# Performance work log

Hardware: AMD Instinct MI355X
Metric: run time of the kernel (lower is better)

## Reference

```python
import jax, jax.numpy as jnp
import numpy as np

NUM_HEADS = 8
QUERY_DIM = 512
VALUE_DIM = 512
INPUT_DIM = 512
Q_HEAD = QUERY_DIM // NUM_HEADS   # 64
V_HEAD = VALUE_DIM // NUM_HEADS   # 64
TOPK = 5
BN_EPS = 1e-5


def setup_inputs() -> dict:
    key = jax.random.key(0)
    ks = jax.random.split(key, 3)
    B = 2048
    x = jax.random.normal(ks[0], (B, INPUT_DIM), dtype=jnp.float32)
    # small init scale so softmax logits are reasonable
    W_qkv = jax.random.normal(ks[1], (INPUT_DIM, 2 * QUERY_DIM + VALUE_DIM), dtype=jnp.float32) * 0.02
    W_proj = jax.random.normal(ks[2], (VALUE_DIM, VALUE_DIM), dtype=jnp.float32) * 0.02
    b_proj = jnp.zeros((VALUE_DIM,), dtype=jnp.float32)
    bn_gamma = jnp.ones((VALUE_DIM,), dtype=jnp.float32)
    bn_beta = jnp.zeros((VALUE_DIM,), dtype=jnp.float32)
    return {"x": x, "W_qkv": W_qkv, "W_proj": W_proj, "b_proj": b_proj,
            "bn_gamma": bn_gamma, "bn_beta": bn_beta}


def _batchnorm_train(y, gamma, beta):
    # torch BatchNorm1d training mode: batch mean, biased variance
    mean = y.mean(axis=0)
    var = y.var(axis=0)  # biased (ddof=0), matches torch normalization
    return gamma * (y - mean) * jax.lax.rsqrt(var + BN_EPS) + beta


def reference(x, W_qkv, W_proj, b_proj, bn_gamma, bn_beta):
    B = x.shape[0]
    # qkv_transform: Linear(input_dim, 2Q + V, bias=False)
    qkv = x @ W_qkv                                   # [B, 2Q+V]
    qv = qkv[:, :2 * QUERY_DIM].reshape(B, 2, NUM_HEADS, Q_HEAD)
    q = qv[:, 0].transpose(1, 0, 2)                   # [H, B, hd]
    k = qv[:, 1].transpose(1, 0, 2)                   # [H, B, hd]
    v = qkv[:, 2 * QUERY_DIM:].reshape(B, NUM_HEADS, V_HEAD).transpose(1, 0, 2)  # [H, B, vd]

    scale = 1.0 / jnp.sqrt(jnp.float32(Q_HEAD))
    logits = jnp.einsum('hqd,hkd->hqk', q, k) * scale  # [H, B, B]
    attn = jax.nn.softmax(logits, axis=-1)

    # per-head: zero the top-5 columns by summed attention weight (no grad through selection)
    col_sums = jax.lax.stop_gradient(attn.sum(axis=1))           # [H, B]
    _, top_idx = jax.lax.top_k(col_sums, TOPK)                   # [H, 5]
    mask = jnp.ones((NUM_HEADS, B), dtype=attn.dtype)
    mask = mask.at[jnp.arange(NUM_HEADS)[:, None], top_idx].set(0.0)
    attn = attn * mask[:, None, :]                               # zero columns

    out = jnp.einsum('hqk,hkd->hqd', attn, v)                    # [H, B, vd]
    out = out.transpose(1, 0, 2).reshape(B, VALUE_DIM)
    # proj: Linear + BatchNorm1d (training mode) + ReLU
    out = out @ W_proj.T + b_proj
    out = jax.nn.relu(_batchnorm_train(out, bn_gamma, bn_beta))
    return out, attn
```

## Files before the change

kernel.cpp:

```cpp
#include <hip/hip_runtime.h>
#include <hip/hip_bf16.h>

#define B 2048
#define NH 8
#define HD 64
#define DIM 512
#define QKVN 1536
#define OUT0_ELEMS ((size_t)B * DIM)

typedef float f32x4 __attribute__((ext_vector_type(4)));
typedef __bf16 bf16x8 __attribute__((ext_vector_type(8)));

static __device__ __forceinline__ unsigned short f2bf(float f) {
    unsigned int u = __builtin_bit_cast(unsigned int, f);
    u += 0x7fffu + ((u >> 16) & 1u);
    return (unsigned short)(u >> 16);
}
static __device__ __forceinline__ float bfhi2f(unsigned int u) {
    return __builtin_bit_cast(float, u & 0xffff0000u);
}
static __device__ __forceinline__ float bflo2f(unsigned int u) {
    return __builtin_bit_cast(float, u << 16);
}

__global__ __launch_bounds__(256) void prep_cast(const float* __restrict__ x,
                                                 const float* __restrict__ wp,
                                                 const float* __restrict__ wqkv,
                                                 unsigned short* __restrict__ xbf,
                                                 unsigned short* __restrict__ wpbf,
                                                 unsigned short* __restrict__ wT) {
    int bx = blockIdx.x;
    int tid = threadIdx.x;
    if (bx < 1280) {
        size_t t = (size_t)bx * 256 + tid;
        const float4* src;
        ushort4* dst;
        size_t idx;
        if (t < 262144) { src = (const float4*)x; dst = (ushort4*)xbf; idx = t; }
        else            { src = (const float4*)wp; dst = (ushort4*)wpbf; idx = t - 262144; }
        float4 v = src[idx];
        ushort4 u;
        u.x = f2bf(v.x); u.y = f2bf(v.y); u.z = f2bf(v.z); u.w = f2bf(v.w);
        dst[idx] = u;
        return;
    }
    int b = bx - 1280;
    int n0 = (b % 24) * 64;
    int k0 = (b / 24) * 64;
    __shared__ unsigned short T[64][72];
#pragma unroll
    for (int it = 0; it < 4; ++it) {
        int chunk = it * 256 + tid;
        int r = chunk >> 4, c4 = (chunk & 15) * 4;
        float4 v = *(const float4*)(wqkv + (size_t)(k0 + r) * QKVN + n0 + c4);
        T[c4 + 0][r] = f2bf(v.x); T[c4 + 1][r] = f2bf(v.y);
        T[c4 + 2][r] = f2bf(v.z); T[c4 + 3][r] = f2bf(v.w);
    }
    __syncthreads();
#pragma unroll
    for (int it = 0; it < 2; ++it) {
        int chunk = it * 256 + tid;
        int r = chunk >> 3, c8 = (chunk & 7) * 8;
        ushort4 u0, u1;
        u0.x = T[r][c8 + 0]; u0.y = T[r][c8 + 1]; u0.z = T[r][c8 + 2]; u0.w = T[r][c8 + 3];
        u1.x = T[r][c8 + 4]; u1.y = T[r][c8 + 5]; u1.z = T[r][c8 + 6]; u1.w = T[r][c8 + 7];
        *(ushort4*)(wT + (size_t)(n0 + r) * 512 + k0 + c8) = u0;
        *(ushort4*)(wT + (size_t)(n0 + r) * 512 + k0 + c8 + 4) = u1;
    }
}

__global__ __launch_bounds__(256) void gemm_qkv_mfma(const unsigned short* __restrict__ xbf,
                                                     const unsigned short* __restrict__ wT,
                                                     float* __restrict__ v_f32,
                                                     unsigned short* __restrict__ qkbf,
                                                     unsigned short* __restrict__ vT) {
    int nt = blockIdx.x;
    int mt = blockIdx.y;
    __shared__ uint4 Ax[128 * 8];
    __shared__ uint4 Bw[64 * 8];
    int tid = threadIdx.x;
    int l = tid & 63, wid = tid >> 6;
    int wr = wid >> 1, wc = wid & 1;
    const uint4* x4 = (const uint4*)xbf;
    const uint4* w4 = (const uint4*)wT;
    f32x4 acc[4][2];
#pragma unroll
    for (int i = 0; i < 4; ++i)
#pragma unroll
        for (int j = 0; j < 2; ++j) acc[i][j] = (f32x4){0.f, 0.f, 0.f, 0.f};

    for (int kt = 0; kt < 8; ++kt) {
        int kg = kt * 8;
#pragma unroll
        for (int it = 0; it < 4; ++it) {
            int chunk = it * 256 + tid;
            int row = chunk >> 3, slot = chunk & 7;
            Ax[row * 8 + (slot ^ (row & 7))] = x4[(size_t)(mt * 128 + row) * 64 + kg + slot];
        }
#pragma unroll
        for (int it = 0; it < 2; ++it) {
            int chunk = it * 256 + tid;
            int row = chunk >> 3, slot = chunk & 7;
            Bw[row * 8 + (slot ^ (row & 7))] = w4[(size_t)(nt * 64 + row) * 64 + kg + slot];
        }
        __syncthreads();
#pragma unroll
        for (int km = 0; km < 2; ++km) {
            int gsel = km * 4 + (l >> 4);
            bf16x8 a[4], b[2];
#pragma unroll
            for (int i = 0; i < 4; ++i) {
                int row = wr * 64 + i * 16 + (l & 15);
                a[i] = __builtin_bit_cast(bf16x8, Ax[row * 8 + (gsel ^ (row & 7))]);
            }
#pragma unroll
            for (int j = 0; j < 2; ++j) {
                int row = wc * 32 + j * 16 + (l & 15);
                b[j] = __builtin_bit_cast(bf16x8, Bw[row * 8 + (gsel ^ (row & 7))]);
            }
#pragma unroll
            for (int i = 0; i < 4; ++i)
#pragma unroll
                for (int j = 0; j < 2; ++j)
                    acc[i][j] = __builtin_amdgcn_mfma_f32_16x16x32_bf16(a[i], b[j], acc[i][j], 0, 0, 0);
        }
        __syncthreads();
    }
    if (nt < 16) {
#pragma unroll
        for (int i = 0; i < 4; ++i)
#pragma unroll
            for (int j = 0; j < 2; ++j)
#pragma unroll
                for (int reg = 0; reg < 4; ++reg) {
                    int row = mt * 128 + wr * 64 + i * 16 + (l >> 4) * 4 + reg;
                    int col = nt * 64 + wc * 32 + j * 16 + (l & 15);
                    qkbf[(size_t)row * 1024 + col] = f2bf(acc[i][j][reg]);
                }
    } else {
        int h = nt - 16;
#pragma unroll
        for (int i = 0; i < 4; ++i)
#pragma unroll
            for (int j = 0; j < 2; ++j) {
                int k0r = mt * 128 + wr * 64 + i * 16 + (l >> 4) * 4;
                int d = wc * 32 + j * 16 + (l & 15);
                uint2 pk;
                pk.x = (unsigned)f2bf(acc[i][j][0]) | ((unsigned)f2bf(acc[i][j][1]) << 16);
                pk.y = (unsigned)f2bf(acc[i][j][2]) | ((unsigned)f2bf(acc[i][j][3]) << 16);
                *(uint2*)(vT + ((size_t)(h * 64 + d) * 2048 + k0r)) = pk;
#pragma unroll
                for (int reg = 0; reg < 4; ++reg)
                    v_f32[(size_t)(k0r + reg) * DIM + h * 64 + d] = acc[i][j][reg];
            }
    }
}

template<int PHASE>
__global__ __launch_bounds__(256) void attn_pass(const unsigned short* __restrict__ qkbf,
                                                 const unsigned short* __restrict__ vT,
                                                 const float* __restrict__ rowsum_in,
                                                 float* __restrict__ rowsum_out,
                                                 float* __restrict__ attn,
                                                 float* __restrict__ colsum,
                                                 float* __restrict__ ovp) {
    int ct = blockIdx.x, qt = blockIdx.y, h = blockIdx.z;
    int tid = threadIdx.x;
    int l = tid & 63;
    int wid = tid >> 6;
    int wr = wid >> 1;
    int wc = wid & 1;

    __shared__ uint4 Qs[128 * 8];
    __shared__ uint4 Ks[64 * 8];
    __shared__ uint4 Vt[64 * 8];
    __shared__ uint4 Pl4[128 * 8];
    __shared__ float cs[512];
    __shared__ float rinv[128];
    unsigned short* Pl = (unsigned short*)Pl4;

    const uint4* src = (const uint4*)qkbf;
#pragma unroll
    for (int it = 0; it < 4; ++it) {
        int chunk = it * 256 + tid;
        int row = chunk >> 3, slot = chunk & 7;
        Qs[row * 8 + (slot ^ (row & 7))] = src[(size_t)(qt * 128 + row) * 128 + h * 8 + slot];
    }
    if constexpr (PHASE == 2) {
        if (tid < 128) rinv[tid] = 1.0f / rowsum_in[h * B + qt * 128 + tid];
        if (tid < 256) { cs[tid] = 0.f; cs[tid + 256] = 0.f; }
    }

    float rsum[4][4];
    f32x4 O[4][2];
    if constexpr (PHASE == 1) {
#pragma unroll
        for (int i = 0; i < 4; ++i)
#pragma unroll
            for (int r = 0; r < 4; ++r) rsum[i][r] = 0.f;
    } else {
#pragma unroll
        for (int i = 0; i < 4; ++i)
#pragma unroll
            for (int j = 0; j < 2; ++j) O[i][j] = (f32x4){0.f, 0.f, 0.f, 0.f};
    }

    size_t hbb = (size_t)h * B * B;
    for (int sub = 0; sub < 8; ++sub) {
        int kbase = ct * 512 + sub * 64;
#pragma unroll
        for (int it = 0; it < 2; ++it) {
            int chunk = it * 256 + tid;
            int row = chunk >> 3, slot = chunk & 7;
            Ks[row * 8 + (slot ^ (row & 7))] = src[(size_t)(kbase + row) * 128 + 64 + h * 8 + slot];
        }
        if constexpr (PHASE == 2) {
#pragma unroll
            for (int it = 0; it < 2; ++it) {
                int chunk = it * 256 + tid;
                int d = chunk >> 3, g = chunk & 7;
                Vt[d * 8 + (g ^ (d & 7))] =
                    *(const uint4*)(vT + ((size_t)(h * 64 + d) * 2048 + kbase + g * 8));
            }
        }
        __syncthreads();

        f32x4 S[4][2];
#pragma unroll
        for (int i = 0; i < 4; ++i)
#pragma unroll
            for (int j = 0; j < 2; ++j) S[i][j] = (f32x4){0.f, 0.f, 0.f, 0.f};
#pragma unroll
        for (int km = 0; km < 2; ++km) {
            int gsel = km * 4 + (l >> 4);
            bf16x8 aq[4], bk[2];
#pragma unroll
            for (int i = 0; i < 4; ++i) {
                int row = wr * 64 + i * 16 + (l & 15);
                aq[i] = __builtin_bit_cast(bf16x8, Qs[row * 8 + (gsel ^ (row & 7))]);
            }
#pragma unroll
            for (int j = 0; j < 2; ++j) {
                int row = wc * 32 + j * 16 + (l & 15);
                bk[j] = __builtin_bit_cast(bf16x8, Ks[row * 8 + (gsel ^ (row & 7))]);
            }
#pragma unroll
            for (int i = 0; i < 4; ++i)
#pragma unroll
                for (int j = 0; j < 2; ++j)
                    S[i][j] = __builtin_amdgcn_mfma_f32_16x16x32_bf16(aq[i], bk[j], S[i][j], 0, 0, 0);
        }

        if constexpr (PHASE == 1) {
#pragma unroll
            for (int i = 0; i < 4; ++i)
#pragma unroll
                for (int j = 0; j < 2; ++j)
#pragma unroll
                    for (int reg = 0; reg < 4; ++reg)
                        rsum[i][reg] += __expf(S[i][j][reg] * 0.125f);
            __syncthreads();
        } else {
            float csacc[2] = {0.f, 0.f};
#pragma unroll
            for (int i = 0; i < 4; ++i) {
#pragma unroll
                for (int j = 0; j < 2; ++j) {
                    int kcol = wc * 32 + j * 16 + (l & 15);
#pragma unroll
                    for (int reg = 0; reg < 4; ++reg) {
                        int qrow = wr * 64 + i * 16 + (l >> 4) * 4 + reg;
                        float p = __expf(S[i][j][reg] * 0.125f) * rinv[qrow];
                        csacc[j] += p;
                        Pl[qrow * 64 + ((kcol & 7) | ((((kcol >> 3) ^ (qrow & 7))) << 3))] = f2bf(p);
                    }
                }
            }
#pragma unroll
            for (int j = 0; j < 2; ++j) {
                float v = csacc[j];
                v += __shfl_xor(v, 16);
                v += __shfl_xor(v, 32);
                if (l < 16) atomicAdd(&cs[sub * 64 + wc * 32 + j * 16 + l], v);
            }
            __syncthreads();
#pragma unroll
            for (int it2 = 0; it2 < 4; ++it2) {
                int chunk = it2 * 256 + tid;
                int row = chunk >> 3, g = chunk & 7;
                uint4 pv = Pl4[row * 8 + (g ^ (row & 7))];
                float4 lo, hi;
                lo.x = bflo2f(pv.x); lo.y = bfhi2f(pv.x);
                lo.z = bflo2f(pv.y); lo.w = bfhi2f(pv.y);
                hi.x = bflo2f(pv.z); hi.y = bfhi2f(pv.z);
                hi.z = bflo2f(pv.w); hi.w = bfhi2f(pv.w);
                float* dst = attn + hbb + (size_t)(qt * 128 + row) * B + kbase + g * 8;
                *(float4*)dst = lo;
                *(float4*)(dst + 4) = hi;
            }
#pragma unroll
            for (int km = 0; km < 2; ++km) {
                int gsel = km * 4 + (l >> 4);
                bf16x8 pa[4], vb[2];
#pragma unroll
                for (int i = 0; i < 4; ++i) {
                    int q = wr * 64 + i * 16 + (l & 15);
                    pa[i] = __builtin_bit_cast(bf16x8, Pl4[q * 8 + (gsel ^ (q & 7))]);
                }
#pragma unroll
                for (int j = 0; j < 2; ++j) {
                    int d = wc * 32 + j * 16 + (l & 15);
                    vb[j] = __builtin_bit_cast(bf16x8, Vt[d * 8 + (gsel ^ (d & 7))]);
                }
#pragma unroll
                for (int i = 0; i < 4; ++i)
#pragma unroll
                    for (int j = 0; j < 2; ++j)
                        O[i][j] = __builtin_amdgcn_mfma_f32_16x16x32_bf16(pa[i], vb[j], O[i][j], 0, 0, 0);
            }
            __syncthreads();
        }
    }

    if constexpr (PHASE == 1) {
#pragma unroll
        for (int i = 0; i < 4; ++i)
#pragma unroll
            for (int reg = 0; reg < 4; ++reg) {
                float v = rsum[i][reg];
                v += __shfl_xor(v, 1); v += __shfl_xor(v, 2);
                v += __shfl_xor(v, 4); v += __shfl_xor(v, 8);
                if ((l & 15) == 0)
                    atomicAdd(&rowsum_out[h * B + qt * 128 + wr * 64 + i * 16 + (l >> 4) * 4 + reg], v);
            }
    } else {
        for (int i = tid; i < 512; i += 256)
            atomicAdd(&colsum[h * B + ct * 512 + i], cs[i]);
#pragma unroll
        for (int i = 0; i < 4; ++i)
#pragma unroll
            for (int j = 0; j < 2; ++j)
#pragma unroll
                for (int reg = 0; reg < 4; ++reg) {
                    int qrow = wr * 64 + i * 16 + (l >> 4) * 4 + reg;
                    ovp[((size_t)ct * B + qt * 128 + qrow) * DIM + h * 64 + wc * 32 + j * 16 + (l & 15)] =
                        O[i][j][reg];
                }
    }
}

__global__ __launch_bounds__(256) void maskfix_topk(float* __restrict__ attn,
                                                    const float* __restrict__ v_f32,
                                                    const float* __restrict__ colsum,
                                                    const float* __restrict__ ovp,
                                                    unsigned short* __restrict__ ovbf) {
    int rt = blockIdx.x;
    int h = blockIdx.y;
    int tid = threadIdx.x;
    __shared__ float v[B];
    __shared__ float bv[256];
    __shared__ int bi[256];
    __shared__ float Pl[5][64];
    __shared__ float Vl[5][64];
    __shared__ int tix[5];
    for (int i = tid; i < B; i += 256) v[i] = colsum[h * B + i];
    __syncthreads();
    for (int it = 0; it < 5; ++it) {
        float best = -1e30f;
        int bidx = 0;
        for (int i = tid; i < B; i += 256) {
            float x = v[i];
            if (x > best || (x == best && i < bidx)) { best = x; bidx = i; }
        }
        bv[tid] = best; bi[tid] = bidx;
        __syncthreads();
        for (int s = 128; s > 0; s >>= 1) {
            if (tid < s) {
                if (bv[tid + s] > bv[tid] ||
                    (bv[tid + s] == bv[tid] && bi[tid + s] < bi[tid])) {
                    bv[tid] = bv[tid + s]; bi[tid] = bi[tid + s];
                }
            }
            __syncthreads();
        }
        if (tid == 0) { tix[it] = bi[0]; v[bi[0]] = -1e30f; }
        __syncthreads();
    }
    size_t abase = (size_t)h * B * B + (size_t)(rt * 64) * B;
    for (int t = tid; t < 320; t += 256) {
        int i = t / 64, q = t % 64;
        Pl[i][q] = attn[abase + (size_t)q * B + tix[i]];
        Vl[i][q] = v_f32[(size_t)tix[i] * DIM + h * 64 + q];
    }
    __syncthreads();
    for (int t = tid; t < 320; t += 256) {
        int i = t / 64, q = t % 64;
        attn[abase + (size_t)q * B + tix[i]] = 0.f;
    }
    int tx = tid % 16, ty = tid / 16;
    float corr[4][4] = {};
#pragma unroll
    for (int i = 0; i < 5; ++i)
#pragma unroll
        for (int a = 0; a < 4; ++a)
#pragma unroll
            for (int b2 = 0; b2 < 4; ++b2)
                corr[a][b2] += Pl[i][ty * 4 + a] * Vl[i][tx * 4 + b2];
#pragma unroll
    for (int a = 0; a < 4; ++a) {
        size_t row = (size_t)(rt * 64 + ty * 4 + a);
        size_t col = h * 64 + tx * 4;
        float4 s0 = *(const float4*)(ovp + ((size_t)0 * B + row) * DIM + col);
        float4 s1 = *(const float4*)(ovp + ((size_t)1 * B + row) * DIM + col);
        float4 s2 = *(const float4*)(ovp + ((size_t)2 * B + row) * DIM + col);
        float4 s3 = *(const float4*)(ovp + ((size_t)3 * B + row) * DIM + col);
        ushort4 u;
        u.x = f2bf(s0.x + s1.x + s2.x + s3.x - corr[a][0]);
        u.y = f2bf(s0.y + s1.y + s2.y + s3.y - corr[a][1]);
        u.z = f2bf(s0.z + s1.z + s2.z + s3.z - corr[a][2]);
        u.w = f2bf(s0.w + s1.w + s2.w + s3.w - corr[a][3]);
        *(ushort4*)(ovbf + row * DIM + col) = u;
    }
}

__global__ __launch_bounds__(256) void proj_gemm_mfma(const unsigned short* __restrict__ ovbf,
                                                      const unsigned short* __restrict__ wpbf,
                                                      const float* __restrict__ bproj,
                                                      float* __restrict__ y,
                                                      float* __restrict__ sums,
                                                      float* __restrict__ ssums) {
    int nt = blockIdx.x;
    int mt = blockIdx.y;
    __shared__ uint4 Ax[128 * 8];
    __shared__ uint4 Bw[64 * 8];
    __shared__ float sb[64];
    __shared__ float qb[64];
    int tid = threadIdx.x;
    int l = tid & 63, wid = tid >> 6;
    int wr = wid >> 1, wc = wid & 1;
    if (tid < 64) { sb[tid] = 0.f; qb[tid] = 0.f; }
    const uint4* a4 = (const uint4*)ovbf;
    const uint4* b4 = (const uint4*)wpbf;
    f32x4 acc[4][2];
#pragma unroll
    for (int i = 0; i < 4; ++i)
#pragma unroll
        for (int j = 0; j < 2; ++j) acc[i][j] = (f32x4){0.f, 0.f, 0.f, 0.f};

    for (int kt = 0; kt < 8; ++kt) {
        int kg = kt * 8;
#pragma unroll
        for (int it = 0; it < 4; ++it) {
            int chunk = it * 256 + tid;
            int row = chunk >> 3, slot = chunk & 7;
            Ax[row * 8 + (slot ^ (row & 7))] = a4[(size_t)(mt * 128 + row) * 64 + kg + slot];
        }
#pragma unroll
        for (int it = 0; it < 2; ++it) {
            int chunk = it * 256 + tid;
            int row = chunk >> 3, slot = chunk & 7;
            Bw[row * 8 + (slot ^ (row & 7))] = b4[(size_t)(nt * 64 + row) * 64 + kg + slot];
        }
        __syncthreads();
#pragma unroll
        for (int km = 0; km < 2; ++km) {
            int gsel = km * 4 + (l >> 4);
            bf16x8 a[4], b[2];
#pragma unroll
            for (int i = 0; i < 4; ++i) {
                int row = wr * 64 + i * 16 + (l & 15);
                a[i] = __builtin_bit_cast(bf16x8, Ax[row * 8 + (gsel ^ (row & 7))]);
            }
#pragma unroll
            for (int j = 0; j < 2; ++j) {
                int row = wc * 32 + j * 16 + (l & 15);
                b[j] = __builtin_bit_cast(bf16x8, Bw[row * 8 + (gsel ^ (row & 7))]);
            }
#pragma unroll
            for (int i = 0; i < 4; ++i)
#pragma unroll
                for (int j = 0; j < 2; ++j)
                    acc[i][j] = __builtin_amdgcn_mfma_f32_16x16x32_bf16(a[i], b[j], acc[i][j], 0, 0, 0);
        }
        __syncthreads();
    }
    float ls[2] = {0.f, 0.f};
    float lq[2] = {0.f, 0.f};
#pragma unroll
    for (int i = 0; i < 4; ++i)
#pragma unroll
        for (int j = 0; j < 2; ++j) {
            int col = nt * 64 + wc * 32 + j * 16 + (l & 15);
            float bp = bproj[col];
#pragma unroll
            for (int reg = 0; reg < 4; ++reg) {
                int row = mt * 128 + wr * 64 + i * 16 + (l >> 4) * 4 + reg;
                float c = acc[i][j][reg] + bp;
                y[(size_t)row * DIM + col] = c;
                ls[j] += c; lq[j] += c * c;
            }
        }
#pragma unroll
    for (int j = 0; j < 2; ++j) {
        atomicAdd(&sb[wc * 32 + j * 16 + (l & 15)], ls[j]);
        atomicAdd(&qb[wc * 32 + j * 16 + (l & 15)], lq[j]);
    }
    __syncthreads();
    if (tid < 64) {
        atomicAdd(&sums[nt * 64 + tid], sb[tid]);
        atomicAdd(&ssums[nt * 64 + tid], qb[tid]);
    }
}

__global__ __launch_bounds__(256) void bn_apply(const float* __restrict__ y,
                                                const float* __restrict__ sums,
                                                const float* __restrict__ ssums,
                                                const float* __restrict__ gamma,
                                                const float* __restrict__ beta,
                                                float* __restrict__ out) {
    int t = blockIdx.x * 256 + threadIdx.x;
    int c4 = (t % 128) * 4;
    size_t r = t / 128;
    if (r >= B) return;
    float4 s = *(const float4*)(sums + c4);
    float4 q = *(const float4*)(ssums + c4);
    float4 m, rs;
    m.x = s.x * (1.0f / B); m.y = s.y * (1.0f / B);
    m.z = s.z * (1.0f / B); m.w = s.w * (1.0f / B);
    rs.x = rsqrtf(q.x * (1.0f / B) - m.x * m.x + 1e-5f);
    rs.y = rsqrtf(q.y * (1.0f / B) - m.y * m.y + 1e-5f);
    rs.z = rsqrtf(q.z * (1.0f / B) - m.z * m.z + 1e-5f);
    rs.w = rsqrtf(q.w * (1.0f / B) - m.w * m.w + 1e-5f);
    float4 v = *(const float4*)(y + r * DIM + c4);
    float4 g = *(const float4*)(gamma + c4);
    float4 bt = *(const float4*)(beta + c4);
    float4 o;
    o.x = fmaxf(0.f, g.x * (v.x - m.x) * rs.x + bt.x);
    o.y = fmaxf(0.f, g.y * (v.y - m.y) * rs.y + bt.y);
    o.z = fmaxf(0.f, g.z * (v.z - m.z) * rs.z + bt.z);
    o.w = fmaxf(0.f, g.w * (v.w - m.w) * rs.w + bt.w);
    *(float4*)(out + r * DIM + c4) = o;
}

extern "C" void kernel_launch(void* const* d_in, const int* in_sizes, int n_in,
                              void* d_out, int out_size, void* d_ws, size_t ws_size,
                              hipStream_t stream) {
    const float* x = (const float*)d_in[0];
    const float* W_qkv = (const float*)d_in[1];
    const float* W_proj = (const float*)d_in[2];
    const float* b_proj = (const float*)d_in[3];
    const float* bn_gamma = (const float*)d_in[4];
    const float* bn_beta = (const float*)d_in[5];

    float* out0 = (float*)d_out;
    float* attn = (float*)d_out + OUT0_ELEMS;

    float* ws = (float*)d_ws;
    float* v_f32 = ws;
    float* ovp = v_f32 + OUT0_ELEMS;
    float* y = ovp + 4 * OUT0_ELEMS;
    float* rowsum = y + OUT0_ELEMS;
    float* colsum = rowsum + NH * B;
    float* sums = colsum + NH * B;
    float* ssums = sums + DIM;
    unsigned short* qkbf = (unsigned short*)(ssums + DIM);
    unsigned short* vT = qkbf + (size_t)B * 1024;
    unsigned short* wpbf = vT + (size_t)NH * HD * B;
    unsigned short* ovbf = wpbf + (size_t)DIM * DIM;
    unsigned short* xbf = (unsigned short*)ovp;
    unsigned short* wT = xbf + (size_t)B * 512;

    hipMemsetAsync(rowsum, 0, (2 * NH * B + 2 * DIM) * sizeof(float), stream);

    prep_cast<<<1280 + 192, 256, 0, stream>>>(x, W_proj, W_qkv, xbf, wpbf, wT);
    gemm_qkv_mfma<<<dim3(QKVN / 64, B / 128), 256, 0, stream>>>(xbf, wT, v_f32, qkbf, vT);
    attn_pass<1><<<dim3(4, 16, NH), 256, 0, stream>>>(qkbf, vT, nullptr, rowsum,
                                                      attn, colsum, ovp);
    attn_pass<2><<<dim3(4, 16, NH), 256, 0, stream>>>(qkbf, vT, rowsum, nullptr,
                                                      attn, colsum, ovp);
    maskfix_topk<<<dim3(B / 64, NH), 256, 0, stream>>>(attn, v_f32, colsum, ovp, ovbf);
    proj_gemm_mfma<<<dim3(DIM / 64, B / 128), 256, 0, stream>>>(ovbf, wpbf, b_proj,
                                                                y, sums, ssums);
    bn_apply<<<(B * DIM / 4 + 255) / 256, 256, 0, stream>>>(y, sums, ssums,
                                                            bn_gamma, bn_beta, out0);
}
```

Before: 104.5 us.

## Split attention passes into finer-grained grids and fold memset into prep kernel

The templated two-phase attention kernel becomes two separate kernels. The rowsum pass now covers 256 key columns per block, doubling its grid. The second pass works on 64-row query tiles with one 16-column slice per wave, doubling that grid and cutting shared memory per block. The zeroing of rowsum/colsum/sums buffers moves from a hipMemsetAsync into extra blocks of prep_cast, saving one launch. More blocks should raise occupancy and fill the GPU better, but K/V tiles are reloaded more often and there are more atomics.

```diff
diff --git a/kernel.cpp b/kernel.cpp
--- a/kernel.cpp
+++ b/kernel.cpp
@@ -28,7 +28,8 @@
                                                  const float* __restrict__ wqkv,
                                                  unsigned short* __restrict__ xbf,
                                                  unsigned short* __restrict__ wpbf,
-                                                 unsigned short* __restrict__ wT) {
+                                                 unsigned short* __restrict__ wT,
+                                                 float* __restrict__ zero_region) {
     int bx = blockIdx.x;
     int tid = threadIdx.x;
     if (bx < 1280) {
@@ -42,6 +43,12 @@
         ushort4 u;
         u.x = f2bf(v.x); u.y = f2bf(v.y); u.z = f2bf(v.z); u.w = f2bf(v.w);
         dst[idx] = u;
+        return;
+    }
+    if (bx >= 1472) {
+        int idx = (bx - 1472) * 256 + tid;
+        if (idx < 8448)
+            ((float4*)zero_region)[idx] = make_float4(0.f, 0.f, 0.f, 0.f);
         return;
     }
     int b = bx - 1280;
@@ -156,14 +163,8 @@
     }
 }
 
-template<int PHASE>
-__global__ __launch_bounds__(256) void attn_pass(const unsigned short* __restrict__ qkbf,
-                                                 const unsigned short* __restrict__ vT,
-                                                 const float* __restrict__ rowsum_in,
-                                                 float* __restrict__ rowsum_out,
-                                                 float* __restrict__ attn,
-                                                 float* __restrict__ colsum,
-                                                 float* __restrict__ ovp) {
+__global__ __launch_bounds__(256) void attn_rowsum(const unsigned short* __restrict__ qkbf,
+                                                   float* __restrict__ rowsum) {
     int ct = blockIdx.x, qt = blockIdx.y, h = blockIdx.z;
     int tid = threadIdx.x;
     int l = tid & 63;
@@ -173,11 +174,6 @@
 
     __shared__ uint4 Qs[128 * 8];
     __shared__ uint4 Ks[64 * 8];
-    __shared__ uint4 Vt[64 * 8];
-    __shared__ uint4 Pl4[128 * 8];
-    __shared__ float cs[512];
-    __shared__ float rinv[128];
-    unsigned short* Pl = (unsigned short*)Pl4;
 
     const uint4* src = (const uint4*)qkbf;
 #pragma unroll
@@ -186,43 +182,21 @@
         int row = chunk >> 3, slot = chunk & 7;
         Qs[row * 8 + (slot ^ (row & 7))] = src[(size_t)(qt * 128 + row) * 128 + h * 8 + slot];
     }
-    if constexpr (PHASE == 2) {
-        if (tid < 128) rinv[tid] = 1.0f / rowsum_in[h * B + qt * 128 + tid];
-        if (tid < 256) { cs[tid] = 0.f; cs[tid + 256] = 0.f; }
-    }
 
     float rsum[4][4];
-    f32x4 O[4][2];
-    if constexpr (PHASE == 1) {
-#pragma unroll
-        for (int i = 0; i < 4; ++i)
-#pragma unroll
-            for (int r = 0; r < 4; ++r) rsum[i][r] = 0.f;
-    } else {
-#pragma unroll
-        for (int i = 0; i < 4; ++i)
-#pragma unroll
-            for (int j = 0; j < 2; ++j) O[i][j] = (f32x4){0.f, 0.f, 0.f, 0.f};
-    }
-
-    size_t hbb = (size_t)h * B * B;
-    for (int sub = 0; sub < 8; ++sub) {
-        int kbase = ct * 512 + sub * 64;
+#pragma unroll
+    for (int i = 0; i < 4; ++i)
+#pragma unroll
+        for (int r = 0; r < 4; ++r) rsum[i][r] = 0.f;
+
+    for (int sub = 0; sub < 4; ++sub) {
+        int kbase = ct * 256 + sub * 64;
 #pragma unroll
         for (int it = 0; it < 2; ++it) {
             int chunk = it * 256 + tid;
             int row = chunk >> 3, slot = chunk & 7;
             Ks[row * 8 + (slot ^ (row & 7))] = src[(size_t)(kbase + row) * 128 + 64 + h * 8 + slot];
         }
-        if constexpr (PHASE == 2) {
-#pragma unroll
-            for (int it = 0; it < 2; ++it) {
-                int chunk = it * 256 + tid;
-                int d = chunk >> 3, g = chunk & 7;
-                Vt[d * 8 + (g ^ (d & 7))] =
-                    *(const uint4*)(vT + ((size_t)(h * 64 + d) * 2048 + kbase + g * 8));
-            }
-        }
         __syncthreads();
 
         f32x4 S[4][2];
@@ -250,103 +224,165 @@
                 for (int j = 0; j < 2; ++j)
                     S[i][j] = __builtin_amdgcn_mfma_f32_16x16x32_bf16(aq[i], bk[j], S[i][j], 0, 0, 0);
         }
-
-        if constexpr (PHASE == 1) {
+#pragma unroll
+        for (int i = 0; i < 4; ++i)
+#pragma unroll
+            for (int j = 0; j < 2; ++j)
+#pragma unroll
+                for (int reg = 0; reg < 4; ++reg)
+                    rsum[i][reg] += __expf(S[i][j][reg] * 0.125f);
+        __syncthreads();
+    }
+
+#pragma unroll
+    for (int i = 0; i < 4; ++i)
+#pragma unroll
+        for (int reg = 0; reg < 4; ++reg) {
+            float v = rsum[i][reg];
+            v += __shfl_xor(v, 1); v += __shfl_xor(v, 2);
+            v += __shfl_xor(v, 4); v += __shfl_xor(v, 8);
+            if ((l & 15) == 0)
+                atomicAdd(&rowsum[h * B + qt * 128 + wr * 64 + i * 16 + (l >> 4) * 4 + reg], v);
+        }
+}
+
+__global__ __launch_bounds__(256) void attn_pass2(const unsigned short* __restrict__ qkbf,
+                                                  const unsigned short* __restrict__ vT,
+                                                  const float* __restrict__ rowsum,
+                                                  float* __restrict__ attn,
+                                                  float* __restrict__ colsum,
+                                                  float* __restrict__ ovp) {
+    int ct = blockIdx.x, qt = blockIdx.y, h = blockIdx.z;
+    int tid = threadIdx.x;
+    int l = tid & 63;
+    int w = tid >> 6;
+
+    __shared__ uint4 Qs[64 * 8];
+    __shared__ uint4 Ks[64 * 8];
+    __shared__ uint4 Vt[64 * 8];
+    __shared__ uint4 Pl4[64 * 8];
+    __shared__ float cs[512];
+    __shared__ float rinv[64];
+    unsigned short* Pl = (unsigned short*)Pl4;
+
+    const uint4* src = (const uint4*)qkbf;
+#pragma unroll
+    for (int it = 0; it < 2; ++it) {
+        int chunk = it * 256 + tid;
+        int row = chunk >> 3, slot = chunk & 7;
+        Qs[row * 8 + (slot ^ (row & 7))] = src[(size_t)(qt * 64 + row) * 128 + h * 8 + slot];
+    }
+    if (tid < 64) rinv[tid] = 1.0f / rowsum[h * B + qt * 64 + tid];
+    if (tid < 256) { cs[tid] = 0.f; cs[tid + 256] = 0.f; }
+
+    f32x4 O[4];
+#pragma unroll
+    for (int i = 0; i < 4; ++i) O[i] = (f32x4){0.f, 0.f, 0.f, 0.f};
+
+    size_t hbb = (size_t)h * B * B;
+    for (int sub = 0; sub < 8; ++sub) {
+        int kbase = ct * 512 + sub * 64;
+#pragma unroll
+        for (int it = 0; it < 2; ++it) {
+            int chunk = it * 256 + tid;
+            int row = chunk >> 3, slot = chunk & 7;
+            Ks[row * 8 + (slot ^ (row & 7))] = src[(size_t)(kbase + row) * 128 + 64 + h * 8 + slot];
+        }
+#pragma unroll
+        for (int it = 0; it < 2; ++it) {
+            int chunk = it * 256 + tid;
+            int d = chunk >> 3, g = chunk & 7;
+            Vt[d * 8 + (g ^ (d & 7))] =
+                *(const uint4*)(vT + ((size_t)(h * 64 + d) * 2048 + kbase + g * 8));
+        }
+        __syncthreads();
+
+        f32x4 S[4];
+#pragma unroll
+        for (int i = 0; i < 4; ++i) S[i] = (f32x4){0.f, 0.f, 0.f, 0.f};
+#pragma unroll
+        for (int km = 0; km < 2; ++km) {
+            int gsel = km * 4 + (l >> 4);
+            bf16x8 aq[4], bk;
+#pragma unroll
+            for (int i = 0; i < 4; ++i) {
+                int row = i * 16 + (l & 15);
+                aq[i] = __builtin_bit_cast(bf16x8, Qs[row * 8 + (gsel ^ (row & 7))]);
+            }
+            {
+                int row = w * 16 + (l & 15);
+                bk = __builtin_bit_cast(bf16x8, Ks[row * 8 + (gsel ^ (row & 7))]);
+            }
 #pragma unroll
             for (int i = 0; i < 4; ++i)
-#pragma unroll
-                for (int j = 0; j < 2; ++j)
-#pragma unroll
-                    for (int reg = 0; reg < 4; ++reg)
-                        rsum[i][reg] += __expf(S[i][j][reg] * 0.125f);
-            __syncthreads();
-        } else {
-            float csacc[2] = {0.f, 0.f};
+                S[i] = __builtin_amdgcn_mfma_f32_16x16x32_bf16(aq[i], bk, S[i], 0, 0, 0);
+        }
+
+        float csacc = 0.f;
+        int kcol = w * 16 + (l & 15);
+#pragma unroll
+        for (int i = 0; i < 4; ++i) {
+#pragma unroll
+            for (int reg = 0; reg < 4; ++reg) {
+                int qrow = i * 16 + (l >> 4) * 4 + reg;
+                float p = __expf(S[i][reg] * 0.125f) * rinv[qrow];
+                csacc += p;
+                Pl[qrow * 64 + ((kcol & 7) | ((((kcol >> 3) ^ (qrow & 7))) << 3))] = f2bf(p);
+            }
+        }
+        {
+            float v = csacc;
+            v += __shfl_xor(v, 16);
+            v += __shfl_xor(v, 32);
+            if (l < 16) atomicAdd(&cs[sub * 64 + w * 16 + l], v);
+        }
+        __syncthreads();
+
+#pragma unroll
+        for (int it2 = 0; it2 < 2; ++it2) {
+            int chunk = it2 * 256 + tid;
+            int row = chunk >> 3, g = chunk & 7;
+            uint4 pv = Pl4[row * 8 + (g ^ (row & 7))];
+            float4 lo, hi;
+            lo.x = bflo2f(pv.x); lo.y = bfhi2f(pv.x);
+            lo.z = bflo2f(pv.y); lo.w = bfhi2f(pv.y);
+            hi.x = bflo2f(pv.z); hi.y = bfhi2f(pv.z);
+            hi.z = bflo2f(pv.w); hi.w = bfhi2f(pv.w);
+            float* dst = attn + hbb + (size_t)(qt * 64 + row) * B + kbase + g * 8;
+            *(float4*)dst = lo;
+            *(float4*)(dst + 4) = hi;
+        }
+
+#pragma unroll
+        for (int km = 0; km < 2; ++km) {
+            int gsel = km * 4 + (l >> 4);
+            bf16x8 pa[4], vb;
 #pragma unroll
             for (int i = 0; i < 4; ++i) {
-#pragma unroll
-                for (int j = 0; j < 2; ++j) {
-                    int kcol = wc * 32 + j * 16 + (l & 15);
-#pragma unroll
-                    for (int reg = 0; reg < 4; ++reg) {
-                        int qrow = wr * 64 + i * 16 + (l >> 4) * 4 + reg;
-                        float p = __expf(S[i][j][reg] * 0.125f) * rinv[qrow];
-                        csacc[j] += p;
-                        Pl[qrow * 64 + ((kcol & 7) | ((((kcol >> 3) ^ (qrow & 7))) << 3))] = f2bf(p);
-                    }
-                }
-            }
-#pragma unroll
-            for (int j = 0; j < 2; ++j) {
-                float v = csacc[j];
-                v += __shfl_xor(v, 16);
-                v += __shfl_xor(v, 32);
-                if (l < 16) atomicAdd(&cs[sub * 64 + wc * 32 + j * 16 + l], v);
-            }
-            __syncthreads();
-#pragma unroll
-            for (int it2 = 0; it2 < 4; ++it2) {
-                int chunk = it2 * 256 + tid;
-                int row = chunk >> 3, g = chunk & 7;
-                uint4 pv = Pl4[row * 8 + (g ^ (row & 7))];
-                float4 lo, hi;
-                lo.x = bflo2f(pv.x); lo.y = bfhi2f(pv.x);
-                lo.z = bflo2f(pv.y); lo.w = bfhi2f(pv.y);
-                hi.x = bflo2f(pv.z); hi.y = bfhi2f(pv.z);
-                hi.z = bflo2f(pv.w); hi.w = bfhi2f(pv.w);
-                float* dst = attn + hbb + (size_t)(qt * 128 + row) * B + kbase + g * 8;
-                *(float4*)dst = lo;
-                *(float4*)(dst + 4) = hi;
-            }
-#pragma unroll
-            for (int km = 0; km < 2; ++km) {
-                int gsel = km * 4 + (l >> 4);
-                bf16x8 pa[4], vb[2];
-#pragma unroll
-                for (int i = 0; i < 4; ++i) {
-                    int q = wr * 64 + i * 16 + (l & 15);
-                    pa[i] = __builtin_bit_cast(bf16x8, Pl4[q * 8 + (gsel ^ (q & 7))]);
-                }
-#pragma unroll
-                for (int j = 0; j < 2; ++j) {
-                    int d = wc * 32 + j * 16 + (l & 15);
-                    vb[j] = __builtin_bit_cast(bf16x8, Vt[d * 8 + (gsel ^ (d & 7))]);
-                }
-#pragma unroll
-                for (int i = 0; i < 4; ++i)
-#pragma unroll
-                    for (int j = 0; j < 2; ++j)
-                        O[i][j] = __builtin_amdgcn_mfma_f32_16x16x32_bf16(pa[i], vb[j], O[i][j], 0, 0, 0);
-            }
-            __syncthreads();
-        }
-    }
-
-    if constexpr (PHASE == 1) {
-#pragma unroll
-        for (int i = 0; i < 4; ++i)
-#pragma unroll
-            for (int reg = 0; reg < 4; ++reg) {
-                float v = rsum[i][reg];
-                v += __shfl_xor(v, 1); v += __shfl_xor(v, 2);
-                v += __shfl_xor(v, 4); v += __shfl_xor(v, 8);
-                if ((l & 15) == 0)
-                    atomicAdd(&rowsum_out[h * B + qt * 128 + wr * 64 + i * 16 + (l >> 4) * 4 + reg], v);
-            }
-    } else {
-        for (int i = tid; i < 512; i += 256)
-            atomicAdd(&colsum[h * B + ct * 512 + i], cs[i]);
-#pragma unroll
-        for (int i = 0; i < 4; ++i)
-#pragma unroll
-            for (int j = 0; j < 2; ++j)
-#pragma unroll
-                for (int reg = 0; reg < 4; ++reg) {
-                    int qrow = wr * 64 + i * 16 + (l >> 4) * 4 + reg;
-                    ovp[((size_t)ct * B + qt * 128 + qrow) * DIM + h * 64 + wc * 32 + j * 16 + (l & 15)] =
-                        O[i][j][reg];
-                }
-    }
+                int q = i * 16 + (l & 15);
+                pa[i] = __builtin_bit_cast(bf16x8, Pl4[q * 8 + (gsel ^ (q & 7))]);
+            }
+            {
+                int d = w * 16 + (l & 15);
+                vb = __builtin_bit_cast(bf16x8, Vt[d * 8 + (gsel ^ (d & 7))]);
+            }
+#pragma unroll
+            for (int i = 0; i < 4; ++i)
+                O[i] = __builtin_amdgcn_mfma_f32_16x16x32_bf16(pa[i], vb, O[i], 0, 0, 0);
+        }
+        __syncthreads();
+    }
+
+    for (int i = tid; i < 512; i += 256)
+        atomicAdd(&colsum[h * B + ct * 512 + i], cs[i]);
+#pragma unroll
+    for (int i = 0; i < 4; ++i)
+#pragma unroll
+        for (int reg = 0; reg < 4; ++reg) {
+            int qrow = i * 16 + (l >> 4) * 4 + reg;
+            ovp[((size_t)ct * B + qt * 64 + qrow) * DIM + h * 64 + w * 16 + (l & 15)] =
+                O[i][reg];
+        }
 }
 
 __global__ __launch_bounds__(256) void maskfix_topk(float* __restrict__ attn,
@@ -570,14 +606,10 @@
     unsigned short* xbf = (unsigned short*)ovp;
     unsigned short* wT = xbf + (size_t)B * 512;
 
-    hipMemsetAsync(rowsum, 0, (2 * NH * B + 2 * DIM) * sizeof(float), stream);
-
-    prep_cast<<<1280 + 192, 256, 0, stream>>>(x, W_proj, W_qkv, xbf, wpbf, wT);
+    prep_cast<<<1280 + 192 + 33, 256, 0, stream>>>(x, W_proj, W_qkv, xbf, wpbf, wT, rowsum);
     gemm_qkv_mfma<<<dim3(QKVN / 64, B / 128), 256, 0, stream>>>(xbf, wT, v_f32, qkbf, vT);
-    attn_pass<1><<<dim3(4, 16, NH), 256, 0, stream>>>(qkbf, vT, nullptr, rowsum,
-                                                      attn, colsum, ovp);
-    attn_pass<2><<<dim3(4, 16, NH), 256, 0, stream>>>(qkbf, vT, rowsum, nullptr,
-                                                      attn, colsum, ovp);
+    attn_rowsum<<<dim3(8, 16, NH), 256, 0, stream>>>(qkbf, rowsum);
+    attn_pass2<<<dim3(4, 32, NH), 256, 0, stream>>>(qkbf, vT, rowsum, attn, colsum, ovp);
     maskfix_topk<<<dim3(B / 64, NH), 256, 0, stream>>>(attn, v_f32, colsum, ovp, ovbf);
     proj_gemm_mfma<<<dim3(DIM / 64, B / 128), 256, 0, stream>>>(ovbf, wpbf, b_proj,
                                                                 y, sums, ssums);
```

Result: slower. 108.5 us (+3.8%).
